# Performance work log

Measured on AMD Instinct MI355X. Metric: run time of the kernel, lower is better.

Reference implementation:

```python
import jax, jax.numpy as jnp
import numpy as np

N = 50000      # num nodes
E = 800000     # num edges
F_IN = 128     # CONFIG.FeatureLen()
H = 100        # conv1_hide
C = 16         # CONFIG.ClassNum()
LEAKY = 0.01


def setup_inputs() -> dict:
    key = jax.random.key(0)
    k = jax.random.split(key, 4)
    x = jax.random.normal(k[0], (N, F_IN), dtype=jnp.float32)
    edge_index = jax.random.randint(k[1], (2, E), 0, N, dtype=jnp.int32)
    W1 = jax.random.normal(k[2], (F_IN, H), dtype=jnp.float32) / np.sqrt(F_IN).astype(np.float32)
    b1 = jnp.zeros((H,), dtype=jnp.float32)
    W2 = jax.random.normal(k[3], (H, C), dtype=jnp.float32) / np.sqrt(H).astype(np.float32)
    b2 = jnp.zeros((C,), dtype=jnp.float32)
    return {"x": x, "W1": W1, "b1": b1, "W2": W2, "b2": b2, "edge_index": edge_index}


def _gcn_conv(x, W, b, src, dst):
    """PyG GCNConv: x' = D^{-1/2}(A+I)D^{-1/2} X W + b (symmetric norm, self-loops)."""
    x = x @ W  # transform first (smaller feature dim for propagation)
    loop = jnp.arange(N, dtype=src.dtype)
    s = jnp.concatenate([src, loop])  # sources (message senders)
    d = jnp.concatenate([dst, loop])  # targets (message receivers)
    deg = jax.ops.segment_sum(jnp.ones_like(d, dtype=x.dtype), d, num_segments=N)
    dinv = jnp.where(deg > 0, jax.lax.rsqrt(deg), 0.0)
    norm = dinv[s] * dinv[d]                      # [E+N]
    msg = x[s] * norm[:, None]                    # gather + scale
    out = jax.ops.segment_sum(msg, d, num_segments=N)  # scatter-add
    return out + b


def reference(x, W1, b1, W2, b2, edge_index):
    src, dst = edge_index[0], edge_index[1]
    h = _gcn_conv(x, W1, b1, src, dst)
    h = jax.nn.leaky_relu(h, negative_slope=LEAKY)
    # dropout is identity in eval mode (training=False)
    h = _gcn_conv(h, W2, b2, src, dst)
    return jax.nn.log_softmax(h, axis=1)
```

## Files before the change

### kernel.cpp

```cpp
#include <hip/hip_runtime.h>

#define F_IN 128
#define HDIM 100
#define HPAD 128
#define CDIM 16
#define CAP  64
#define NB   32
#define BT_STRIDE 136
#define CHUNK 4096
#define KMAX 1600
#define RCAP 24

static constexpr float LEAKY = 0.01f;

using short8  = __attribute__((ext_vector_type(8))) short;
using float4v = __attribute__((ext_vector_type(4))) float;
using float2v = __attribute__((ext_vector_type(2))) float;

__device__ __forceinline__ unsigned short f2bf(float f) {
    unsigned u = __float_as_uint(f);
    u += 0x7fffu + ((u >> 16) & 1u);
    return (unsigned short)(u >> 16);
}


__global__ __launch_bounds__(256) void k_gemm1_p1(const float* __restrict__ x,
                                                  const float* __restrict__ W1,
                                                  unsigned char* __restrict__ y1f8,
                                                  const int* __restrict__ src,
                                                  const int* __restrict__ dst,
                                                  unsigned* __restrict__ bkt_edges,
                                                  int* __restrict__ cnt_arr,
                                                  int N, int E, int FB, int KBKT) {
    __shared__ union {
        unsigned short bt[F_IN * BT_STRIDE];
        struct { unsigned stage[CHUNK]; int cnt[KMAX]; } p1;
    } sm;
    int bx = blockIdx.x;
    int t = threadIdx.x;

    if (bx < FB) {
        unsigned* stage = sm.p1.stage;
        int* cnt = sm.p1.cnt;
        for (int i = t; i < KBKT; i += 256) cnt[i] = 0;
        __syncthreads();
        int e0 = bx * CHUNK, e1 = min(E, e0 + CHUNK);
        for (int i = e0 + t; i < e1; i += 256) {
            int d = dst[i];
            unsigned pk = ((unsigned)d << 16) | (unsigned)src[i];
            atomicAdd(&cnt[d >> 5], 1);
            stage[i - e0] = pk;
        }
        __syncthreads();
        for (int i = t; i < KBKT; i += 256) cnt_arr[bx * KBKT + i] = cnt[i];
        __syncthreads();
        for (int i = t; i < KBKT; i += 256) cnt[i] = 0;
        __syncthreads();
        int m = e1 - e0;
        for (int i = t; i < m; i += 256) {
            unsigned pk = stage[i];
            int b = pk >> 21;
            int pos = atomicAdd(&cnt[b], 1);
            if (pos < RCAP)
                bkt_edges[((size_t)b * FB + bx) * RCAP + pos] = pk;
        }
        return;
    }

    for (int idx = t; idx < F_IN * HPAD; idx += 256) {
        int k = idx >> 7;
        int n = idx & 127;
        float v = (n < HDIM) ? W1[k * HDIM + n] : 0.f;
        sm.bt[n * BT_STRIDE + k] = f2bf(v);
    }
    __syncthreads();

    int wave = t >> 6, lane = t & 63;
    int Mtiles = (N + 15) >> 4;
    int tile = (bx - FB) * 4 + wave;
    if (tile >= Mtiles) return;
    int row0 = tile * 16;

    int m = lane & 15;
    int kq = lane >> 4;
    int arow = min(row0 + m, N - 1);
    const float* xrow = x + (size_t)arow * F_IN;

    short8 afrag[4];
    #pragma unroll
    for (int kt = 0; kt < 4; ++kt) {
        int kb = kt * 32 + kq * 8;
        float4 a0 = *(const float4*)(xrow + kb);
        float4 a1 = *(const float4*)(xrow + kb + 4);
        short8 f;
        f[0] = (short)f2bf(a0.x); f[1] = (short)f2bf(a0.y);
        f[2] = (short)f2bf(a0.z); f[3] = (short)f2bf(a0.w);
        f[4] = (short)f2bf(a1.x); f[5] = (short)f2bf(a1.y);
        f[6] = (short)f2bf(a1.z); f[7] = (short)f2bf(a1.w);
        afrag[kt] = f;
    }

    bool full = (row0 + 15 < N);
    #pragma unroll
    for (int ct = 0; ct < 8; ++ct) {
        float4v acc = {0.f, 0.f, 0.f, 0.f};
        #pragma unroll
        for (int kt = 0; kt < 4; ++kt) {
            short8 b = *(const short8*)&sm.bt[(ct * 16 + m) * BT_STRIDE + kt * 32 + kq * 8];
            acc = __builtin_amdgcn_mfma_f32_16x16x32_bf16(afrag[kt], b, acc, 0, 0, 0);
        }
        #pragma unroll
        for (int i = 0; i < 4; ++i) {
            int r = row0 + kq * 4 + i;
            int v8 = __builtin_amdgcn_cvt_pk_fp8_f32(acc[i], acc[i], 0, false);
            if (full || r < N)
                y1f8[(size_t)r * HPAD + ct * 16 + m] = (unsigned char)(v8 & 0xff);
        }
    }
}


__global__ __launch_bounds__(256) void k_deg2(const unsigned* __restrict__ bkt_edges,
                                              const int* __restrict__ cnt_arr,
                                              int* __restrict__ deg,
                                              int N, int FB, int KBKT) {
    __shared__ int cur[NB];
    int b = blockIdx.x, t = threadIdx.x;
    if (t < NB) cur[t] = 0;
    __syncthreads();
    for (int fb = t; fb < FB; fb += 256) {
        int c = min(cnt_arr[fb * KBKT + b], RCAP);
        size_t base = ((size_t)b * FB + fb) * RCAP;
        for (int j = 0; j < c; ++j) {
            unsigned pk = bkt_edges[base + j];
            atomicAdd(&cur[(pk >> 16) & (NB - 1)], 1);
        }
    }
    __syncthreads();
    int n = b * NB + t;
    if (t < NB && n < N) deg[n] = cur[t];
}


__global__ __launch_bounds__(256) void k_agg1y2(const unsigned* __restrict__ y1u,
                                                const float* __restrict__ b1,
                                                const float* __restrict__ W2,
                                                const int* __restrict__ deg,
                                                const unsigned* __restrict__ bkt_edges,
                                                const int* __restrict__ cnt_arr,
                                                float* __restrict__ y2,
                                                int N, int FB, int KBKT) {
    __shared__ float W2s[HDIM * CDIM];
    __shared__ float b1s[HPAD];
    __shared__ float hs[4][2][HPAD];
    __shared__ unsigned short slotsL[NB * CAP];
    __shared__ int cur[NB];
    int b = blockIdx.x, t = threadIdx.x;
    int n0 = b * NB;

    for (int idx = t; idx < HDIM * CDIM; idx += 256) W2s[idx] = W2[idx];
    if (t < HPAD) b1s[t] = (t < HDIM) ? b1[t] : 0.f;
    if (t < NB) cur[t] = 0;
    __syncthreads();

    for (int fb = t; fb < FB; fb += 256) {
        int c = min(cnt_arr[fb * KBKT + b], RCAP);
        size_t base = ((size_t)b * FB + fb) * RCAP;
        for (int j = 0; j < c; ++j) {
            unsigned pk = bkt_edges[base + j];
            int loc = (pk >> 16) & (NB - 1);
            int pos = atomicAdd(&cur[loc], 1);
            if (pos < CAP)
                slotsL[loc * CAP + pos] = (unsigned short)(pk & 0xffffu);
        }
    }
    __syncthreads();

    int wave = t >> 6, lane = t & 63;
    int half = lane >> 5, l = lane & 31;
    int hbase = lane & 32;
    for (int pass = 0; pass < 4; ++pass) {
        int loc = pass * 8 + wave * 2 + half;
        int n = n0 + loc;
        bool valid = (n < N);
        int nn = valid ? n : (N - 1);
        int cnt = cur[loc];
        float dn = rsqrtf((float)cnt + 1.0f);

        int cother = __shfl(cnt, lane ^ 32);
        int cmax = max(cnt, cother);

        float a0 = 0.f, a1 = 0.f, a2 = 0.f, a3 = 0.f;
        for (int e0 = 0; e0 < cmax; e0 += 32) {
            int mm = min(32, cnt - e0);
            unsigned su = 0u; float wv = 0.f;
            if (l < mm) {
                su = slotsL[loc * CAP + e0 + l];
                wv = rsqrtf((float)deg[su] + 1.0f);
            }
            int mmax = min(32, cmax - e0);
            int mpad = (mmax + 7) & ~7;
            for (int j = 0; j < mpad; j += 8) {
                float w[8]; unsigned vv[8];
                #pragma unroll
                for (int q = 0; q < 8; ++q) {
                    int ln = hbase | (j + q);
                    unsigned s = (unsigned)__shfl((int)su, ln);
                    w[q] = __shfl(wv, ln);
                    vv[q] = y1u[(size_t)s * 32 + l];
                }
                #pragma unroll
                for (int q = 0; q < 8; ++q) {
                    float2v lov = __builtin_amdgcn_cvt_pk_f32_fp8((int)vv[q], false);
                    float2v hiv = __builtin_amdgcn_cvt_pk_f32_fp8((int)vv[q], true);
                    a0 = fmaf(w[q], lov[0], a0);
                    a1 = fmaf(w[q], lov[1], a1);
                    a2 = fmaf(w[q], hiv[0], a2);
                    a3 = fmaf(w[q], hiv[1], a3);
                }
            }
        }
        {
            unsigned vn = y1u[(size_t)nn * 32 + l];
            float2v lov = __builtin_amdgcn_cvt_pk_f32_fp8((int)vn, false);
            float2v hiv = __builtin_amdgcn_cvt_pk_f32_fp8((int)vn, true);
            a0 = fmaf(dn, lov[0], a0);
            a1 = fmaf(dn, lov[1], a1);
            a2 = fmaf(dn, hiv[0], a2);
            a3 = fmaf(dn, hiv[1], a3);
        }
        float4 bb = (l < 25) ? *(const float4*)&b1s[4 * l] : make_float4(0.f, 0.f, 0.f, 0.f);
        float h0 = fmaf(dn, a0, bb.x);
        float h1 = fmaf(dn, a1, bb.y);
        float h2 = fmaf(dn, a2, bb.z);
        float h3 = fmaf(dn, a3, bb.w);
        h0 = h0 > 0.f ? h0 : LEAKY * h0;
        h1 = h1 > 0.f ? h1 : LEAKY * h1;
        h2 = h2 > 0.f ? h2 : LEAKY * h2;
        h3 = h3 > 0.f ? h3 : LEAKY * h3;
        *(float4*)&hs[wave][half][4 * l] = make_float4(h0, h1, h2, h3);
        __builtin_amdgcn_wave_barrier();

        int c = l & 15, kg = l >> 4;
        const float* hrow = hs[wave][half];
        float p = 0.f;
        #pragma unroll 10
        for (int j = 0; j < 50; ++j) {
            int k = 2 * j + kg;
            p = fmaf(hrow[k], W2s[k * CDIM + c], p);
        }
        p += __shfl_down(p, 16);
        if (l < 16 && valid) y2[(size_t)n * CDIM + c] = p;
    }
}


__global__ __launch_bounds__(256) void k_agg2(const float* __restrict__ y2,
                                              const float* __restrict__ b2,
                                              const int* __restrict__ deg,
                                              const unsigned* __restrict__ bkt_edges,
                                              const int* __restrict__ cnt_arr,
                                              float* __restrict__ out,
                                              int N, int FB, int KBKT) {
    __shared__ unsigned short slotsL[NB * CAP];
    __shared__ int cur[NB];
    int b = blockIdx.x, t = threadIdx.x;
    int n0 = b * NB;
    if (t < NB) cur[t] = 0;
    __syncthreads();

    for (int fb = t; fb < FB; fb += 256) {
        int c = min(cnt_arr[fb * KBKT + b], RCAP);
        size_t base = ((size_t)b * FB + fb) * RCAP;
        for (int j = 0; j < c; ++j) {
            unsigned pk = bkt_edges[base + j];
            int loc = (pk >> 16) & (NB - 1);
            int pos = atomicAdd(&cur[loc], 1);
            if (pos < CAP)
                slotsL[loc * CAP + pos] = (unsigned short)(pk & 0xffffu);
        }
    }
    __syncthreads();

    int wave = t >> 6, lane = t & 63;
    int sub = lane >> 4, c = lane & 15;
    float b2c = b2[c];
    for (int pass = 0; pass < 2; ++pass) {
        int loc = pass * 16 + wave * 4 + sub;
        int n = n0 + loc;
        bool valid = (n < N);
        int nn = valid ? n : 0;
        int cnt = valid ? cur[loc] : 0;
        float dn = rsqrtf((float)cur[loc] + 1.0f);
        float acc = dn * y2[(size_t)nn * CDIM + c];

        for (int e0 = 0; e0 < cnt; e0 += 16) {
            int mm = min(16, cnt - e0);
            unsigned su = 0u; float wv = 0.f;
            if (c < mm) {
                su = slotsL[loc * CAP + e0 + c];
                wv = rsqrtf((float)deg[su] + 1.0f);
            }
            int mpad = (mm + 3) & ~3;
            for (int j = 0; j < mpad; j += 4) {
                float w[4]; float v[4];
                #pragma unroll
                for (int q = 0; q < 4; ++q) {
                    int ln = (sub << 4) + j + q;
                    unsigned s = (unsigned)__shfl((int)su, ln);
                    w[q] = __shfl(wv, ln);
                    v[q] = y2[(size_t)s * CDIM + c];
                }
                #pragma unroll
                for (int q = 0; q < 4; ++q) acc = fmaf(w[q], v[q], acc);
            }
        }

        float lg = fmaf(dn, acc, b2c);
        float mx = lg;
        #pragma unroll
        for (int k = 8; k; k >>= 1) mx = fmaxf(mx, __shfl_xor(mx, k));
        float ex = __expf(lg - mx);
        #pragma unroll
        for (int k = 8; k; k >>= 1) ex += __shfl_xor(ex, k);
        float lse = mx + __logf(ex);
        if (valid) out[(size_t)n * CDIM + c] = lg - lse;
    }
}


extern "C" void kernel_launch(void* const* d_in, const int* in_sizes, int n_in,
                              void* d_out, int out_size, void* d_ws, size_t ws_size,
                              hipStream_t stream) {
    const float* x  = (const float*)d_in[0];
    const float* W1 = (const float*)d_in[1];
    const float* b1 = (const float*)d_in[2];
    const float* W2 = (const float*)d_in[3];
    const float* b2 = (const float*)d_in[4];
    const int*   ei = (const int*)d_in[5];

    int N = in_sizes[0] / F_IN;
    int E = in_sizes[5] / 2;
    const int* src = ei;
    const int* dst = ei + E;

    int KBKT = (N + NB - 1) / NB;
    int FB   = (E + CHUNK - 1) / CHUNK;

    char* ws = (char*)d_ws;
    size_t off = 0;
    auto alloc = [&](size_t bytes) {
        char* p = ws + off;
        off += (bytes + 255) & ~(size_t)255;
        return p;
    };
    int*            deg       = (int*)alloc((size_t)N * 4);
    unsigned char*  y1f8      = (unsigned char*)alloc((size_t)N * HPAD);
    float*          y2        = (float*)alloc((size_t)N * CDIM * 4);
    int*            cnt_arr   = (int*)alloc((size_t)FB * KBKT * 4);
    unsigned*       bkt_edges = (unsigned*)alloc((size_t)KBKT * FB * RCAP * 4);
    (void)ws_size; (void)n_in; (void)out_size;

    int Mtiles = (N + 15) / 16;
    int GG = (Mtiles + 3) / 4;

    k_gemm1_p1<<<FB + GG, 256, 0, stream>>>(x, W1, y1f8, src, dst,
                                            bkt_edges, cnt_arr, N, E, FB, KBKT);
    k_deg2<<<KBKT, 256, 0, stream>>>(bkt_edges, cnt_arr, deg, N, FB, KBKT);
    k_agg1y2<<<KBKT, 256, 0, stream>>>((const unsigned*)y1f8, b1, W2, deg,
                                       bkt_edges, cnt_arr, y2, N, FB, KBKT);
    k_agg2<<<KBKT, 256, 0, stream>>>(y2, b2, deg, bkt_edges, cnt_arr,
                                     (float*)d_out, N, FB, KBKT);
}
```

Before: 171.6 us.

## Build per-node adjacency once, precompute dinv, pack FP8 GEMM stores

The bucketing kernel now scatters edges in a single pass without an LDS staging buffer. A new k_p2 kernel builds the per-node source-slot lists once, writes them to global memory along with degrees and precomputed rsqrt weights. Both aggregation kernels then load the prebuilt slot lists instead of re-bucketing from bkt_edges, and pair each slot with its dinv value in LDS, which removes the shuffle-based broadcast of indices and weights. The layer-1 GEMM permutes W1 columns so each lane packs four FP8 outputs into a single 32-bit store. The cost is an extra global buffer plus one extra write and read of the slot lists, and edges no longer keep their order within a bucket.

Measured after the change: 167.6 us. -2.3%, faster.

```diff
diff --git a/kernel.cpp b/kernel.cpp
--- a/kernel.cpp
+++ b/kernel.cpp
@@ -34,44 +34,36 @@
                                                   int N, int E, int FB, int KBKT) {
     __shared__ union {
         unsigned short bt[F_IN * BT_STRIDE];
-        struct { unsigned stage[CHUNK]; int cnt[KMAX]; } p1;
+        int p1cnt[KMAX];
     } sm;
     int bx = blockIdx.x;
     int t = threadIdx.x;
 
     if (bx < FB) {
-        unsigned* stage = sm.p1.stage;
-        int* cnt = sm.p1.cnt;
+        int* cnt = sm.p1cnt;
         for (int i = t; i < KBKT; i += 256) cnt[i] = 0;
         __syncthreads();
         int e0 = bx * CHUNK, e1 = min(E, e0 + CHUNK);
         for (int i = e0 + t; i < e1; i += 256) {
             int d = dst[i];
             unsigned pk = ((unsigned)d << 16) | (unsigned)src[i];
-            atomicAdd(&cnt[d >> 5], 1);
-            stage[i - e0] = pk;
-        }
-        __syncthreads();
-        for (int i = t; i < KBKT; i += 256) cnt_arr[bx * KBKT + i] = cnt[i];
-        __syncthreads();
-        for (int i = t; i < KBKT; i += 256) cnt[i] = 0;
-        __syncthreads();
-        int m = e1 - e0;
-        for (int i = t; i < m; i += 256) {
-            unsigned pk = stage[i];
-            int b = pk >> 21;
+            int b = d >> 5;
             int pos = atomicAdd(&cnt[b], 1);
             if (pos < RCAP)
                 bkt_edges[((size_t)b * FB + bx) * RCAP + pos] = pk;
         }
+        __syncthreads();
+        for (int i = t; i < KBKT; i += 256) cnt_arr[bx * KBKT + i] = cnt[i];
         return;
     }
 
     for (int idx = t; idx < F_IN * HPAD; idx += 256) {
         int k = idx >> 7;
-        int n = idx & 127;
-        float v = (n < HDIM) ? W1[k * HDIM + n] : 0.f;
-        sm.bt[n * BT_STRIDE + k] = f2bf(v);
+        int c = idx & 127;
+        int g = c >> 6, r = c & 63, j = r & 3, mm = r >> 2;
+        int slot = (g * 4 + j) * 16 + mm;
+        float v = (c < HDIM) ? W1[k * HDIM + c] : 0.f;
+        sm.bt[slot * BT_STRIDE + k] = f2bf(v);
     }
     __syncthreads();
 
@@ -102,67 +94,43 @@
 
     bool full = (row0 + 15 < N);
     #pragma unroll
-    for (int ct = 0; ct < 8; ++ct) {
-        float4v acc = {0.f, 0.f, 0.f, 0.f};
-        #pragma unroll
-        for (int kt = 0; kt < 4; ++kt) {
-            short8 b = *(const short8*)&sm.bt[(ct * 16 + m) * BT_STRIDE + kt * 32 + kq * 8];
-            acc = __builtin_amdgcn_mfma_f32_16x16x32_bf16(afrag[kt], b, acc, 0, 0, 0);
+    for (int g = 0; g < 2; ++g) {
+        float4v acc[4];
+        #pragma unroll
+        for (int j = 0; j < 4; ++j) acc[j] = (float4v){0.f, 0.f, 0.f, 0.f};
+        #pragma unroll
+        for (int j = 0; j < 4; ++j) {
+            #pragma unroll
+            for (int kt = 0; kt < 4; ++kt) {
+                short8 b = *(const short8*)&sm.bt[((g * 4 + j) * 16 + m) * BT_STRIDE
+                                                  + kt * 32 + kq * 8];
+                acc[j] = __builtin_amdgcn_mfma_f32_16x16x32_bf16(afrag[kt], b, acc[j], 0, 0, 0);
+            }
         }
         #pragma unroll
         for (int i = 0; i < 4; ++i) {
             int r = row0 + kq * 4 + i;
-            int v8 = __builtin_amdgcn_cvt_pk_fp8_f32(acc[i], acc[i], 0, false);
+            int u = __builtin_amdgcn_cvt_pk_fp8_f32(acc[0][i], acc[1][i], 0, false);
+            u = __builtin_amdgcn_cvt_pk_fp8_f32(acc[2][i], acc[3][i], u, true);
             if (full || r < N)
-                y1f8[(size_t)r * HPAD + ct * 16 + m] = (unsigned char)(v8 & 0xff);
-        }
-    }
-}
-
-
-__global__ __launch_bounds__(256) void k_deg2(const unsigned* __restrict__ bkt_edges,
-                                              const int* __restrict__ cnt_arr,
-                                              int* __restrict__ deg,
-                                              int N, int FB, int KBKT) {
+                *(unsigned*)&y1f8[(size_t)r * HPAD + g * 64 + 4 * m] = (unsigned)u;
+        }
+    }
+}
+
+
+__global__ __launch_bounds__(256) void k_p2(const unsigned* __restrict__ bkt_edges,
+                                            const int* __restrict__ cnt_arr,
+                                            int* __restrict__ deg,
+                                            float* __restrict__ dinv,
+                                            unsigned* __restrict__ slots16g,
+                                            int N, int FB, int KBKT) {
+    __shared__ unsigned short slotsL[NB * CAP];
     __shared__ int cur[NB];
     int b = blockIdx.x, t = threadIdx.x;
     if (t < NB) cur[t] = 0;
-    __syncthreads();
-    for (int fb = t; fb < FB; fb += 256) {
-        int c = min(cnt_arr[fb * KBKT + b], RCAP);
-        size_t base = ((size_t)b * FB + fb) * RCAP;
-        for (int j = 0; j < c; ++j) {
-            unsigned pk = bkt_edges[base + j];
-            atomicAdd(&cur[(pk >> 16) & (NB - 1)], 1);
-        }
-    }
-    __syncthreads();
-    int n = b * NB + t;
-    if (t < NB && n < N) deg[n] = cur[t];
-}
-
-
-__global__ __launch_bounds__(256) void k_agg1y2(const unsigned* __restrict__ y1u,
-                                                const float* __restrict__ b1,
-                                                const float* __restrict__ W2,
-                                                const int* __restrict__ deg,
-                                                const unsigned* __restrict__ bkt_edges,
-                                                const int* __restrict__ cnt_arr,
-                                                float* __restrict__ y2,
-                                                int N, int FB, int KBKT) {
-    __shared__ float W2s[HDIM * CDIM];
-    __shared__ float b1s[HPAD];
-    __shared__ float hs[4][2][HPAD];
-    __shared__ unsigned short slotsL[NB * CAP];
-    __shared__ int cur[NB];
-    int b = blockIdx.x, t = threadIdx.x;
-    int n0 = b * NB;
-
-    for (int idx = t; idx < HDIM * CDIM; idx += 256) W2s[idx] = W2[idx];
-    if (t < HPAD) b1s[t] = (t < HDIM) ? b1[t] : 0.f;
-    if (t < NB) cur[t] = 0;
-    __syncthreads();
-
+    for (int i = t; i < NB * CAP / 2; i += 256) ((unsigned*)slotsL)[i] = 0u;
+    __syncthreads();
     for (int fb = t; fb < FB; fb += 256) {
         int c = min(cnt_arr[fb * KBKT + b], RCAP);
         size_t base = ((size_t)b * FB + fb) * RCAP;
@@ -175,10 +143,47 @@
         }
     }
     __syncthreads();
+    for (int i = t; i < NB * CAP / 2; i += 256)
+        slots16g[(size_t)b * (NB * CAP / 2) + i] = ((const unsigned*)slotsL)[i];
+    int n = b * NB + t;
+    if (t < NB && n < N) {
+        deg[n] = cur[t];
+        dinv[n] = rsqrtf((float)cur[t] + 1.0f);
+    }
+}
+
+
+__global__ __launch_bounds__(256) void k_agg1y2(const unsigned* __restrict__ y1u,
+                                                const float* __restrict__ b1,
+                                                const float* __restrict__ W2,
+                                                const int* __restrict__ deg,
+                                                const float* __restrict__ dinv,
+                                                const unsigned short* __restrict__ slots16g,
+                                                float* __restrict__ y2,
+                                                int N, int FB, int KBKT) {
+    __shared__ float W2s[HDIM * CDIM];
+    __shared__ float b1s[HPAD];
+    __shared__ float hs[4][2][HPAD];
+    __shared__ uint2 slotsP[NB * CAP];
+    __shared__ int cur[NB];
+    int b = blockIdx.x, t = threadIdx.x;
+    int n0 = b * NB;
+
+    for (int idx = t; idx < HDIM * CDIM; idx += 256) W2s[idx] = W2[idx];
+    if (t < HPAD) b1s[t] = (t < HDIM) ? b1[t] : 0.f;
+    if (t < NB) cur[t] = (n0 + t < N) ? deg[n0 + t] : 0;
+    __syncthreads();
+
+    for (int i = t; i < NB * CAP; i += 256) {
+        int loc = i >> 6, j = i & 63;
+        unsigned s = slots16g[(size_t)b * (NB * CAP) + i];
+        float w = (j < cur[loc]) ? dinv[s] : 0.f;
+        slotsP[i] = make_uint2(s, __float_as_uint(w));
+    }
+    __syncthreads();
 
     int wave = t >> 6, lane = t & 63;
     int half = lane >> 5, l = lane & 31;
-    int hbase = lane & 32;
     for (int pass = 0; pass < 4; ++pass) {
         int loc = pass * 8 + wave * 2 + half;
         int n = n0 + loc;
@@ -187,37 +192,21 @@
         int cnt = cur[loc];
         float dn = rsqrtf((float)cnt + 1.0f);
 
-        int cother = __shfl(cnt, lane ^ 32);
-        int cmax = max(cnt, cother);
-
         float a0 = 0.f, a1 = 0.f, a2 = 0.f, a3 = 0.f;
-        for (int e0 = 0; e0 < cmax; e0 += 32) {
-            int mm = min(32, cnt - e0);
-            unsigned su = 0u; float wv = 0.f;
-            if (l < mm) {
-                su = slotsL[loc * CAP + e0 + l];
-                wv = rsqrtf((float)deg[su] + 1.0f);
-            }
-            int mmax = min(32, cmax - e0);
-            int mpad = (mmax + 7) & ~7;
-            for (int j = 0; j < mpad; j += 8) {
-                float w[8]; unsigned vv[8];
-                #pragma unroll
-                for (int q = 0; q < 8; ++q) {
-                    int ln = hbase | (j + q);
-                    unsigned s = (unsigned)__shfl((int)su, ln);
-                    w[q] = __shfl(wv, ln);
-                    vv[q] = y1u[(size_t)s * 32 + l];
-                }
-                #pragma unroll
-                for (int q = 0; q < 8; ++q) {
-                    float2v lov = __builtin_amdgcn_cvt_pk_f32_fp8((int)vv[q], false);
-                    float2v hiv = __builtin_amdgcn_cvt_pk_f32_fp8((int)vv[q], true);
-                    a0 = fmaf(w[q], lov[0], a0);
-                    a1 = fmaf(w[q], lov[1], a1);
-                    a2 = fmaf(w[q], hiv[0], a2);
-                    a3 = fmaf(w[q], hiv[1], a3);
-                }
+        int mpad = (cnt + 3) & ~3;
+        const uint2* sp = &slotsP[loc * CAP];
+        for (int e = 0; e < mpad; e += 4) {
+            #pragma unroll
+            for (int q = 0; q < 4; ++q) {
+                uint2 pk = sp[e + q];
+                float w = __uint_as_float(pk.y);
+                unsigned vv = y1u[(size_t)pk.x * 32 + l];
+                float2v lov = __builtin_amdgcn_cvt_pk_f32_fp8((int)vv, false);
+                float2v hiv = __builtin_amdgcn_cvt_pk_f32_fp8((int)vv, true);
+                a0 = fmaf(w, lov[0], a0);
+                a1 = fmaf(w, lov[1], a1);
+                a2 = fmaf(w, hiv[0], a2);
+                a3 = fmaf(w, hiv[1], a3);
             }
         }
         {
@@ -258,27 +247,21 @@
 __global__ __launch_bounds__(256) void k_agg2(const float* __restrict__ y2,
                                               const float* __restrict__ b2,
                                               const int* __restrict__ deg,
-                                              const unsigned* __restrict__ bkt_edges,
-                                              const int* __restrict__ cnt_arr,
+                                              const float* __restrict__ dinv,
+                                              const unsigned short* __restrict__ slots16g,
                                               float* __restrict__ out,
                                               int N, int FB, int KBKT) {
-    __shared__ unsigned short slotsL[NB * CAP];
+    __shared__ uint2 slotsP[NB * CAP];
     __shared__ int cur[NB];
     int b = blockIdx.x, t = threadIdx.x;
     int n0 = b * NB;
-    if (t < NB) cur[t] = 0;
-    __syncthreads();
-
-    for (int fb = t; fb < FB; fb += 256) {
-        int c = min(cnt_arr[fb * KBKT + b], RCAP);
-        size_t base = ((size_t)b * FB + fb) * RCAP;
-        for (int j = 0; j < c; ++j) {
-            unsigned pk = bkt_edges[base + j];
-            int loc = (pk >> 16) & (NB - 1);
-            int pos = atomicAdd(&cur[loc], 1);
-            if (pos < CAP)
-                slotsL[loc * CAP + pos] = (unsigned short)(pk & 0xffffu);
-        }
+    if (t < NB) cur[t] = (n0 + t < N) ? deg[n0 + t] : 0;
+    __syncthreads();
+    for (int i = t; i < NB * CAP; i += 256) {
+        int loc = i >> 6, j = i & 63;
+        unsigned s = slots16g[(size_t)b * (NB * CAP) + i];
+        float w = (j < cur[loc]) ? dinv[s] : 0.f;
+        slotsP[i] = make_uint2(s, __float_as_uint(w));
     }
     __syncthreads();
 
@@ -290,29 +273,19 @@
         int n = n0 + loc;
         bool valid = (n < N);
         int nn = valid ? n : 0;
-        int cnt = valid ? cur[loc] : 0;
-        float dn = rsqrtf((float)cur[loc] + 1.0f);
+        int cnt = cur[loc];
+        float dn = rsqrtf((float)cnt + 1.0f);
         float acc = dn * y2[(size_t)nn * CDIM + c];
 
-        for (int e0 = 0; e0 < cnt; e0 += 16) {
-            int mm = min(16, cnt - e0);
-            unsigned su = 0u; float wv = 0.f;
-            if (c < mm) {
-                su = slotsL[loc * CAP + e0 + c];
-                wv = rsqrtf((float)deg[su] + 1.0f);
-            }
-            int mpad = (mm + 3) & ~3;
-            for (int j = 0; j < mpad; j += 4) {
-                float w[4]; float v[4];
-                #pragma unroll
-                for (int q = 0; q < 4; ++q) {
-                    int ln = (sub << 4) + j + q;
-                    unsigned s = (unsigned)__shfl((int)su, ln);
-                    w[q] = __shfl(wv, ln);
-                    v[q] = y2[(size_t)s * CDIM + c];
-                }
-                #pragma unroll
-                for (int q = 0; q < 4; ++q) acc = fmaf(w[q], v[q], acc);
+        int mpad = (cnt + 3) & ~3;
+        const uint2* sp = &slotsP[loc * CAP];
+        for (int e = 0; e < mpad; e += 4) {
+            #pragma unroll
+            for (int q = 0; q < 4; ++q) {
+                uint2 pk = sp[e + q];
+                float w = __uint_as_float(pk.y);
+                float v = y2[(size_t)pk.x * CDIM + c];
+                acc = fmaf(w, v, acc);
             }
         }
 
@@ -355,10 +328,12 @@
         return p;
     };
     int*            deg       = (int*)alloc((size_t)N * 4);
+    float*          dinv      = (float*)alloc((size_t)N * 4);
     unsigned char*  y1f8      = (unsigned char*)alloc((size_t)N * HPAD);
     float*          y2        = (float*)alloc((size_t)N * CDIM * 4);
     int*            cnt_arr   = (int*)alloc((size_t)FB * KBKT * 4);
     unsigned*       bkt_edges = (unsigned*)alloc((size_t)KBKT * FB * RCAP * 4);
+    unsigned*       slots16g  = (unsigned*)alloc((size_t)KBKT * NB * CAP * 2);
     (void)ws_size; (void)n_in; (void)out_size;
 
     int Mtiles = (N + 15) / 16;
@@ -366,9 +341,10 @@
 
     k_gemm1_p1<<<FB + GG, 256, 0, stream>>>(x, W1, y1f8, src, dst,
                                             bkt_edges, cnt_arr, N, E, FB, KBKT);
-    k_deg2<<<KBKT, 256, 0, stream>>>(bkt_edges, cnt_arr, deg, N, FB, KBKT);
-    k_agg1y2<<<KBKT, 256, 0, stream>>>((const unsigned*)y1f8, b1, W2, deg,
-                                       bkt_edges, cnt_arr, y2, N, FB, KBKT);
-    k_agg2<<<KBKT, 256, 0, stream>>>(y2, b2, deg, bkt_edges, cnt_arr,
+    k_p2<<<KBKT, 256, 0, stream>>>(bkt_edges, cnt_arr, deg, dinv, slots16g, N, FB, KBKT);
+    k_agg1y2<<<KBKT, 256, 0, stream>>>((const unsigned*)y1f8, b1, W2, deg, dinv,
+                                       (const unsigned short*)slots16g, y2, N, FB, KBKT);
+    k_agg2<<<KBKT, 256, 0, stream>>>(y2, b2, deg, dinv,
+                                     (const unsigned short*)slots16g,
                                      (float*)d_out, N, FB, KBKT);
 }
```
